# Optimization experiments

Measured on AMD Instinct MI355X. Metric: run time of the kernel, lower is better.

Reference implementation:

```python
import jax, jax.numpy as jnp
from jax import lax
import numpy as np

B, T, D, H = 64, 512, 1024, 1024

def _lstm_layer(x_tbd, mask_tb, W, U, b):
    """Keras-style LSTM over time-major x (T,B,D). Gate order i,f,g,o.
    Masked timesteps carry previous h,c (Keras mask semantics)."""
    Bsz = x_tbd.shape[1]
    Hsz = U.shape[0]
    # precompute input projection once: (T,B,4H)
    xz = jnp.einsum('tbd,dh->tbh', x_tbd, W) + b

    def step(carry, inp):
        h, c = carry
        zx, m = inp
        z = zx + h @ U
        i, f, g, o = jnp.split(z, 4, axis=-1)
        i = jax.nn.sigmoid(i)
        f = jax.nn.sigmoid(f)
        g = jnp.tanh(g)
        o = jax.nn.sigmoid(o)
        c_new = f * c + i * g
        h_new = o * jnp.tanh(c_new)
        m = m[:, None]
        h2 = jnp.where(m, h_new, h)
        c2 = jnp.where(m, c_new, c)
        return (h2, c2), h2

    h0 = jnp.zeros((Bsz, Hsz), x_tbd.dtype)
    c0 = jnp.zeros((Bsz, Hsz), x_tbd.dtype)
    (h, c), hs = lax.scan(step, (h0, c0), (xz, mask_tb))
    return hs, h, c


def setup_inputs() -> dict:
    key = jax.random.key(0)
    ks = jax.random.split(key, 8)
    sD = 1.0 / np.sqrt(D)
    sH = 1.0 / np.sqrt(H)
    x = jax.random.normal(ks[0], (B, T, D), dtype=jnp.float32)
    lengths = jax.random.randint(ks[1], (B,), 1, T + 1, dtype=jnp.int32)
    # Keras unit_forget_bias: bias zeros except forget gate slice = 1
    b = jnp.zeros((4 * H,), jnp.float32).at[H:2 * H].set(1.0)
    return {
        'x': x,
        'lengths': lengths,
        'W0': jax.random.normal(ks[2], (D, 4 * H), dtype=jnp.float32) * sD,
        'U0': jax.random.normal(ks[3], (H, 4 * H), dtype=jnp.float32) * sH,
        'b0': b,
        'W1': jax.random.normal(ks[4], (H, 4 * H), dtype=jnp.float32) * sH,
        'U1': jax.random.normal(ks[5], (H, 4 * H), dtype=jnp.float32) * sH,
        'b1': b,
    }


def reference(x, lengths, W0, U0, b0, W1, U1, b1):
    Tlen = x.shape[1]
    mask = jnp.arange(Tlen)[None, :] < lengths[:, None]  # (B,T)
    mask_tb = mask.T  # (T,B)
    x_tbd = jnp.transpose(x, (1, 0, 2))  # time-major
    out0, _, _ = _lstm_layer(x_tbd, mask_tb, W0, U0, b0)
    out1, h, c = _lstm_layer(out0, mask_tb, W1, U1, b1)
    rnnout = jnp.transpose(out1, (1, 0, 2))  # (B,T,H)
    return rnnout, h, c
```

## Files before the change

kernel.cpp:

```cpp
#include <hip/hip_runtime.h>
#include <hip/hip_bf16.h>


#define NTT 512

typedef __attribute__((ext_vector_type(8))) short short8;
typedef __attribute__((ext_vector_type(4))) float floatx4;
typedef __attribute__((ext_vector_type(4))) unsigned short ushort4v;
typedef unsigned long long ull;

#define LDS_TOTAL 90112

#define AT_LD(p) __hip_atomic_load((p), __ATOMIC_RELAXED, __HIP_MEMORY_SCOPE_AGENT)
#define AT_ST(p, v) __hip_atomic_store((p), (v), __ATOMIC_RELAXED, __HIP_MEMORY_SCOPE_AGENT)
#define AT_ADD(p, v) __hip_atomic_fetch_add((p), (v), __ATOMIC_RELAXED, __HIP_MEMORY_SCOPE_AGENT)

__device__ __forceinline__ unsigned short f2bf(float f) {
  unsigned int u = __float_as_uint(f);
  u += 0x7fffu + ((u >> 16) & 1u);
  return (unsigned short)(u >> 16);
}
__device__ __forceinline__ float sigmf(float x) { return 1.0f / (1.0f + __expf(-x)); }
__device__ __forceinline__ float tanhfa(float x) { return 1.0f - 2.0f / (1.0f + __expf(2.0f * x)); }

__device__ __forceinline__ void fullbar(ull* base, int bid) {
  __syncthreads();
  if (threadIdx.x == 0) {
    const int l = bid & 7;
    ull* la = base + 16 + 16 * l;
    ull* bc = base + 144 + 16 * l;
    __builtin_amdgcn_fence(__ATOMIC_RELEASE, "agent");
    AT_ADD(la, 1ull);
    if (bid < 8) {
      while (AT_LD(la) < 32ull) __builtin_amdgcn_s_sleep(1);
      AT_ADD(base, 1ull);
      while (AT_LD(base) < 8ull) __builtin_amdgcn_s_sleep(1);
      AT_ST(bc, 1ull);
    } else {
      while (AT_LD(bc) < 1ull) __builtin_amdgcn_s_sleep(1);
    }
    __builtin_amdgcn_fence(__ATOMIC_ACQUIRE, "agent");
  }
  __syncthreads();
}

__device__ __forceinline__ void layer_arrive(ull* base, int sub, ull t1) {
  asm volatile("s_waitcnt vmcnt(0)" ::: "memory");
  __syncthreads();
  if (threadIdx.x == 0) {
    const int l = sub & 7;
    ull* la = base + 16 + 16 * l;
    AT_ADD(la, 1ull);
    if (sub < 8) {
      while (AT_LD(la) < t1 * 16ull) __builtin_amdgcn_s_sleep(1);
      AT_ADD(base, 1ull);
      while (AT_LD(base) < t1 * 8ull) __builtin_amdgcn_s_sleep(1);
      AT_ST(base + 144 + 16 * sub, t1);
    }
  }
}

__device__ __forceinline__ void wait2(ull* own, long long ot, ull* oth, long long xt, int sub) {
  if (threadIdx.x == 0) {
    const int l = sub & 7;
    if (ot > 0)
      while (AT_LD(own + 144 + 16 * l) < (ull)ot) __builtin_amdgcn_s_sleep(1);
    if (xt > 0)
      while (AT_LD(oth + 144 + 16 * l) < (ull)xt) __builtin_amdgcn_s_sleep(1);
  }
  __syncthreads();
}

template <bool COH>
__device__ __forceinline__ short8 ldfrag(const char* p) {
  if constexpr (COH) {
    union { short8 s; ull q[2]; } u;
    u.q[0] = AT_LD((const ull*)p);
    u.q[1] = AT_LD((const ull*)(p + 8));
    return u.s;
  } else {
    return *(const short8*)p;
  }
}

template <bool COH>
__device__ __forceinline__ void ringfill(const char* const* aPm, short8 (*af)[4]) {
#pragma unroll
  for (int kt = 0; kt < 8; ++kt)
#pragma unroll
    for (int mt = 0; mt < 4; ++mt) af[kt][mt] = ldfrag<COH>(aPm[mt] + kt * 64);
}

template <bool COH>
__device__ __forceinline__ void kmain(const char* const* aPm, short8 (*af)[4],
                                      const short8 (*bfr)[2], floatx4 (*acc)[2]) {
#pragma unroll
  for (int kt = 0; kt < 16; ++kt) {
#pragma unroll
    for (int mt = 0; mt < 4; ++mt)
#pragma unroll
      for (int nt = 0; nt < 2; ++nt)
        acc[mt][nt] = __builtin_amdgcn_mfma_f32_16x16x32_bf16(
            af[kt & 7][mt], bfr[kt][nt], acc[mt][nt], 0, 0, 0);
    if (kt < 8) {
#pragma unroll
      for (int mt = 0; mt < 4; ++mt)
        af[kt & 7][mt] = ldfrag<COH>(aPm[mt] + (kt + 8) * 64);
    }
  }
}

__global__ __launch_bounds__(256, 1) void lstm2_persist(
    const float* __restrict__ xin, const int* __restrict__ lens,
    const float* __restrict__ W0, const float* __restrict__ U0, const float* __restrict__ b0v,
    const float* __restrict__ W1, const float* __restrict__ U1, const float* __restrict__ b1v,
    float* __restrict__ out, ull* __restrict__ ws) {
  extern __shared__ char smem[];
  float* red = (float*)smem;

  ull* bar0 = ws;
  ull* bar1 = ws + 512;
  ull* fbar = ws + 1024;
  unsigned short* hbufs = (unsigned short*)(ws + 2048);

  const int tid = threadIdx.x;
  const int bid = blockIdx.x;
  const int layer = bid >> 7;
  const int sub = bid & 127;
  const int hc0 = sub * 8;
  const int wave = tid >> 6;
  const int lane = tid & 63;
  const int c16 = lane & 15;
  const int rowgrp = lane >> 4;

  unsigned short* h0r[4] = {hbufs, hbufs + 65536, hbufs + 131072, hbufs + 196608};
  unsigned short* h1r[2] = {hbufs + 262144, hbufs + 327680};

  const unsigned int gid = (unsigned int)bid * 256u + (unsigned int)tid;
  for (unsigned int i = gid; i < 196608u; i += 65536u) ((unsigned int*)hbufs)[i] = 0u;
  {
    const floatx4* xs = (const floatx4*)xin;
    for (unsigned int q = gid; q < 8388608u; q += 65536u) {
      unsigned int d4 = q & 255u;
      unsigned int bt = q >> 8;
      floatx4 v = xs[q];
      ushort4v o;
      o.x = f2bf(v.x); o.y = f2bf(v.y); o.z = f2bf(v.z); o.w = f2bf(v.w);
      *((ushort4v*)((char*)out + (size_t)bt * 4096) + d4) = o;
    }
  }
  const float* Wm = layer ? W1 : W0;
  const float* Um = layer ? U1 : U0;
  const float* Bsrc = (wave < 2) ? Wm : Um;
  const int kbase = (wave & 1) * 512;
  short8 bf[16][2];
#pragma unroll
  for (int kt = 0; kt < 16; ++kt)
#pragma unroll
    for (int nt = 0; nt < 2; ++nt) {
      const int zc = (nt * 2 + (c16 >> 3)) * 1024 + hc0 + (c16 & 7);
      const float* col = Bsrc + (size_t)(kbase + kt * 32 + rowgrp * 8) * 4096 + zc;
      short8 v;
#pragma unroll
      for (int j = 0; j < 8; ++j) v[j] = (short)f2bf(col[(size_t)j * 4096]);
      bf[kt][nt] = v;
    }
  const float* bv = layer ? b1v : b0v;
  const float bias0 = bv[(c16 >> 3) * 1024 + hc0 + (c16 & 7)];
  const float bias1 = bv[(2 + (c16 >> 3)) * 1024 + hc0 + (c16 & 7)];
  int lens4[4];
#pragma unroll
  for (int r = 0; r < 4; ++r) lens4[r] = lens[wave * 16 + rowgrp * 4 + r];

  fullbar(fbar, bid);

  float hst[4] = {0.f, 0.f, 0.f, 0.f};
  float cst[4] = {0.f, 0.f, 0.f, 0.f};
  const int col = hc0 + c16;

#pragma unroll 1
  for (int t = 0; t < NTT; ++t) {
    const char* aPm[4];
    short8 af[8][4];
    bool isX;
    {
      const char* base0;
      size_t pitch;
      if (layer == 0) {
        if (wave < 2) { base0 = (const char*)out + (size_t)t * 4096 + (size_t)wave * 1024;
                        pitch = (size_t)NTT * 4096; isX = true; }
        else          { base0 = (const char*)h0r[(t + 3) & 3] + (size_t)(wave - 2) * 1024;
                        pitch = 2048; isX = false; }
      } else {
        if (wave < 2) { base0 = (const char*)h0r[t & 3] + (size_t)wave * 1024; }
        else          { base0 = (const char*)h1r[(t + 1) & 1] + (size_t)(wave - 2) * 1024; }
        pitch = 2048; isX = false;
      }
      const char* aP = base0 + (size_t)c16 * pitch + (size_t)rowgrp * 16;
#pragma unroll
      for (int mt = 0; mt < 4; ++mt) aPm[mt] = aP + (size_t)mt * 16 * pitch;
    }

    if (isX) ringfill<false>(aPm, af);

    if (layer == 0) wait2(bar0, t, bar1, (long long)t - 3, sub);
    else            wait2(bar1, t, bar0, (long long)t + 1, sub);

    floatx4 acc[4][2];
#pragma unroll
    for (int mt = 0; mt < 4; ++mt)
#pragma unroll
      for (int nt = 0; nt < 2; ++nt) { floatx4 z = {0.f, 0.f, 0.f, 0.f}; acc[mt][nt] = z; }

    if (isX) {
      kmain<false>(aPm, af, bf, acc);
    } else {
      ringfill<true>(aPm, af);
      kmain<true>(aPm, af, bf, acc);
    }

#pragma unroll
    for (int mt = 0; mt < 4; ++mt)
      if (mt != wave) {
        int slot = mt * 3 + wave - (wave > mt ? 1 : 0);
        *(floatx4*)&red[((slot * 2 + 0) * 64 + lane) * 4] = acc[mt][0];
        *(floatx4*)&red[((slot * 2 + 1) * 64 + lane) * 4] = acc[mt][1];
      }
    __syncthreads();
    floatx4 z0 = acc[wave][0], z1 = acc[wave][1];
#pragma unroll
    for (int q = 0; q < 3; ++q) {
      int slot = wave * 3 + q;
      z0 += *(const floatx4*)&red[((slot * 2 + 0) * 64 + lane) * 4];
      z1 += *(const floatx4*)&red[((slot * 2 + 1) * 64 + lane) * 4];
    }
    z0 += bias0;
    z1 += bias1;

    unsigned short* hW = layer ? h1r[t & 1] : h0r[t & 3];

#pragma unroll
    for (int r = 0; r < 4; ++r) {
      float zi = z0[r], zg = z1[r];
      float zf = __shfl_xor(zi, 8);
      float zo = __shfl_xor(zg, 8);
      float h2, hu_f = 0.f;
      unsigned short hu = 0;
      if (c16 < 8) {
        float ig = sigmf(zi), fg = sigmf(zf), gg = tanhfa(zg), og = sigmf(zo);
        float cn = fg * cst[r] + ig * gg;
        float hn = og * tanhfa(cn);
        bool m = t < lens4[r];
        h2 = m ? hn : hst[r];
        float c2 = m ? cn : cst[r];
        hst[r] = h2;
        cst[r] = c2;
        hu = f2bf(h2);
        hu_f = h2;
      }
      unsigned int up = __shfl_xor((unsigned int)hu, 1);
      float hp = __shfl_xor(hu_f, 1);
      if (c16 < 8 && !(c16 & 1)) {
        int b = wave * 16 + rowgrp * 4 + r;
        unsigned int w = (unsigned int)hu | (up << 16);
        AT_ST((unsigned int*)(hW + b * 1024 + col), w);
        if (layer) {
          float2 f2 = make_float2(hu_f, hp);
          *(float2*)&out[((size_t)b * 512 + (size_t)t) * 1024 + col] = f2;
        }
      }
    }

    if (layer == 0) layer_arrive(bar0, sub, (ull)(t + 1));
    else            layer_arrive(bar1, sub, (ull)(t + 1));
  }

  if (layer && c16 < 8) {
#pragma unroll
    for (int r = 0; r < 4; ++r) {
      int b = wave * 16 + rowgrp * 4 + r;
      out[(size_t)33554432 + (size_t)b * 1024 + col] = hst[r];
      out[(size_t)33554432 + 65536 + (size_t)b * 1024 + col] = cst[r];
    }
  }
}

extern "C" void kernel_launch(void* const* d_in, const int* in_sizes, int n_in,
                              void* d_out, int out_size, void* d_ws, size_t ws_size,
                              hipStream_t stream) {
  (void)in_sizes; (void)n_in; (void)out_size; (void)ws_size;
  const float* x  = (const float*)d_in[0];
  const int* lens = (const int*)d_in[1];
  const float* W0 = (const float*)d_in[2];
  const float* U0 = (const float*)d_in[3];
  const float* b0 = (const float*)d_in[4];
  const float* W1 = (const float*)d_in[5];
  const float* U1 = (const float*)d_in[6];
  const float* b1 = (const float*)d_in[7];

  (void)hipFuncSetAttribute((const void*)lstm2_persist,
                            hipFuncAttributeMaxDynamicSharedMemorySize, LDS_TOTAL);
  hipMemsetAsync(d_ws, 0, 16384, stream);

  lstm2_persist<<<dim3(256), dim3(256), LDS_TOTAL, stream>>>(
      x, lens, W0, U0, b0, W1, U1, b1, (float*)d_out, (ull*)d_ws);
}
```

Baseline: 10.56 ms.

## Merge block pairs into 512-thread blocks and flatten grid barrier to leaf counters

Each workgroup now holds two 256-thread sub-tiles, so 128 blocks (64 per layer) run instead of 256. The two-level tree barrier with a root and broadcast flags is replaced by leaf counters only: arriving blocks increment a leaf, and waiters poll all 8 leaves and take the minimum. The output store for layer 1 moves after the barrier arrive so it leaves the critical path. This aims to cut barrier latency and serialization through the root, at the cost of 8 atomic loads per poll and a heavier per-block register budget under launch_bounds(512,2).

After: 23.99 ms. 127% more time.

```diff
diff --git a/kernel.cpp b/kernel.cpp
--- a/kernel.cpp
+++ b/kernel.cpp
@@ -23,50 +23,43 @@
 __device__ __forceinline__ float sigmf(float x) { return 1.0f / (1.0f + __expf(-x)); }
 __device__ __forceinline__ float tanhfa(float x) { return 1.0f - 2.0f / (1.0f + __expf(2.0f * x)); }
 
-__device__ __forceinline__ void fullbar(ull* base, int bid) {
+__device__ __forceinline__ void fullbar(ull* fb) {
   __syncthreads();
   if (threadIdx.x == 0) {
-    const int l = bid & 7;
-    ull* la = base + 16 + 16 * l;
-    ull* bc = base + 144 + 16 * l;
     __builtin_amdgcn_fence(__ATOMIC_RELEASE, "agent");
-    AT_ADD(la, 1ull);
-    if (bid < 8) {
-      while (AT_LD(la) < 32ull) __builtin_amdgcn_s_sleep(1);
-      AT_ADD(base, 1ull);
-      while (AT_LD(base) < 8ull) __builtin_amdgcn_s_sleep(1);
-      AT_ST(bc, 1ull);
-    } else {
-      while (AT_LD(bc) < 1ull) __builtin_amdgcn_s_sleep(1);
-    }
+    AT_ADD(fb, 1ull);
+    while (AT_LD(fb) < 128ull) __builtin_amdgcn_s_sleep(1);
     __builtin_amdgcn_fence(__ATOMIC_ACQUIRE, "agent");
   }
   __syncthreads();
 }
 
-__device__ __forceinline__ void layer_arrive(ull* base, int sub, ull t1) {
+__device__ __forceinline__ void layer_arrive(ull* base, int sub64) {
   asm volatile("s_waitcnt vmcnt(0)" ::: "memory");
   __syncthreads();
+  if (threadIdx.x == 0) AT_ADD(base + 16 + 16 * (sub64 & 7), 1ull);
+}
+
+__device__ __forceinline__ ull leafmin(const ull* base) {
+  ull v[8];
+#pragma unroll
+  for (int l = 0; l < 8; ++l) v[l] = AT_LD(base + 16 + 16 * l);
+  ull m = v[0];
+#pragma unroll
+  for (int l = 1; l < 8; ++l) m = v[l] < m ? v[l] : m;
+  return m;
+}
+
+__device__ __forceinline__ void wait2(const ull* own, long long ot, const ull* oth, long long xt) {
   if (threadIdx.x == 0) {
-    const int l = sub & 7;
-    ull* la = base + 16 + 16 * l;
-    AT_ADD(la, 1ull);
-    if (sub < 8) {
-      while (AT_LD(la) < t1 * 16ull) __builtin_amdgcn_s_sleep(1);
-      AT_ADD(base, 1ull);
-      while (AT_LD(base) < t1 * 8ull) __builtin_amdgcn_s_sleep(1);
-      AT_ST(base + 144 + 16 * sub, t1);
-    }
-  }
-}
-
-__device__ __forceinline__ void wait2(ull* own, long long ot, ull* oth, long long xt, int sub) {
-  if (threadIdx.x == 0) {
-    const int l = sub & 7;
-    if (ot > 0)
-      while (AT_LD(own + 144 + 16 * l) < (ull)ot) __builtin_amdgcn_s_sleep(1);
-    if (xt > 0)
-      while (AT_LD(oth + 144 + 16 * l) < (ull)xt) __builtin_amdgcn_s_sleep(1);
+    if (ot > 0) {
+      const ull tgt = 8ull * (ull)ot;
+      while (leafmin(own) < tgt) __builtin_amdgcn_s_sleep(1);
+    }
+    if (xt > 0) {
+      const ull tgt = 8ull * (ull)xt;
+      while (leafmin(oth) < tgt) __builtin_amdgcn_s_sleep(1);
+    }
   }
   __syncthreads();
 }
@@ -110,13 +103,12 @@
   }
 }
 
-__global__ __launch_bounds__(256, 1) void lstm2_persist(
+__global__ __launch_bounds__(512, 2) void lstm2_persist(
     const float* __restrict__ xin, const int* __restrict__ lens,
     const float* __restrict__ W0, const float* __restrict__ U0, const float* __restrict__ b0v,
     const float* __restrict__ W1, const float* __restrict__ U1, const float* __restrict__ b1v,
     float* __restrict__ out, ull* __restrict__ ws) {
   extern __shared__ char smem[];
-  float* red = (float*)smem;
 
   ull* bar0 = ws;
   ull* bar1 = ws + 512;
@@ -125,10 +117,14 @@
 
   const int tid = threadIdx.x;
   const int bid = blockIdx.x;
-  const int layer = bid >> 7;
-  const int sub = bid & 127;
+  const int half = tid >> 8;
+  float* red = (float*)(smem + half * 24576);
+
+  const int layer = bid >> 6;
+  const int sub64 = bid & 63;
+  const int sub = sub64 * 2 + half;
   const int hc0 = sub * 8;
-  const int wave = tid >> 6;
+  const int wave = (tid >> 6) & 3;
   const int lane = tid & 63;
   const int c16 = lane & 15;
   const int rowgrp = lane >> 4;
@@ -136,7 +132,7 @@
   unsigned short* h0r[4] = {hbufs, hbufs + 65536, hbufs + 131072, hbufs + 196608};
   unsigned short* h1r[2] = {hbufs + 262144, hbufs + 327680};
 
-  const unsigned int gid = (unsigned int)bid * 256u + (unsigned int)tid;
+  const unsigned int gid = (unsigned int)bid * 512u + (unsigned int)tid;
   for (unsigned int i = gid; i < 196608u; i += 65536u) ((unsigned int*)hbufs)[i] = 0u;
   {
     const floatx4* xs = (const floatx4*)xin;
@@ -172,7 +168,7 @@
 #pragma unroll
   for (int r = 0; r < 4; ++r) lens4[r] = lens[wave * 16 + rowgrp * 4 + r];
 
-  fullbar(fbar, bid);
+  fullbar(fbar);
 
   float hst[4] = {0.f, 0.f, 0.f, 0.f};
   float cst[4] = {0.f, 0.f, 0.f, 0.f};
@@ -203,8 +199,8 @@
 
     if (isX) ringfill<false>(aPm, af);
 
-    if (layer == 0) wait2(bar0, t, bar1, (long long)t - 3, sub);
-    else            wait2(bar1, t, bar0, (long long)t + 1, sub);
+    if (layer == 0) wait2(bar0, t, bar1, (long long)t - 3);
+    else            wait2(bar1, t, bar0, (long long)t + 1);
 
     floatx4 acc[4][2];
 #pragma unroll
@@ -238,6 +234,7 @@
     z1 += bias1;
 
     unsigned short* hW = layer ? h1r[t & 1] : h0r[t & 3];
+    float2 f2s[4];
 
 #pragma unroll
     for (int r = 0; r < 4; ++r) {
@@ -264,15 +261,20 @@
         int b = wave * 16 + rowgrp * 4 + r;
         unsigned int w = (unsigned int)hu | (up << 16);
         AT_ST((unsigned int*)(hW + b * 1024 + col), w);
-        if (layer) {
-          float2 f2 = make_float2(hu_f, hp);
-          *(float2*)&out[((size_t)b * 512 + (size_t)t) * 1024 + col] = f2;
-        }
-      }
-    }
-
-    if (layer == 0) layer_arrive(bar0, sub, (ull)(t + 1));
-    else            layer_arrive(bar1, sub, (ull)(t + 1));
+        f2s[r] = make_float2(hu_f, hp);
+      }
+    }
+
+    if (layer == 0) layer_arrive(bar0, sub64);
+    else            layer_arrive(bar1, sub64);
+
+    if (layer && c16 < 8 && !(c16 & 1)) {
+#pragma unroll
+      for (int r = 0; r < 4; ++r) {
+        int b = wave * 16 + rowgrp * 4 + r;
+        *(float2*)&out[((size_t)b * 512 + (size_t)t) * 1024 + col] = f2s[r];
+      }
+    }
   }
 
   if (layer && c16 < 8) {
@@ -302,6 +304,6 @@
                             hipFuncAttributeMaxDynamicSharedMemorySize, LDS_TOTAL);
   hipMemsetAsync(d_ws, 0, 16384, stream);
 
-  lstm2_persist<<<dim3(256), dim3(256), LDS_TOTAL, stream>>>(
+  lstm2_persist<<<dim3(128), dim3(512), LDS_TOTAL, stream>>>(
       x, lens, W0, U0, b0, W1, U1, b1, (float*)d_out, (ull*)d_ws);
 }
```
